# Kernel optimization log

Hardware: AMD Instinct MI355X
Metric: run time of the kernel (lower is better)

Reference implementation:

```python
import jax, jax.numpy as jnp
import numpy as np

N, D = 16384, 2048


def setup_inputs() -> dict:
    key = jax.random.key(0)
    k1, k2, k3, k4 = jax.random.split(key, 4)
    X = jax.random.normal(k1, (N, D), dtype=jnp.float32)
    keep = jax.random.uniform(k4, (N, D)) > 0.5
    X = jnp.where(keep, X, 0.0)
    A = jax.random.normal(k2, (D, D), dtype=jnp.float32)
    b = jax.random.normal(k3, (D,), dtype=jnp.float32)
    return {"X": X, "A": A, "b": b}


def reference(X, A, b):
    # y_pred = X @ A.T + b
    y_pred = jnp.einsum('nd,kd->nk', X, A) + b  # [N, D]
    mask = X != 0
    masked = jnp.where(mask, y_pred, 0.0)
    row_sum = masked.sum(axis=1, keepdims=True)          # [N, 1]
    has_any = mask.any(axis=1, keepdims=True)            # [N, 1]
    y_out = jnp.where(mask, masked / row_sum, 0.0)
    # rows with an empty mask stay all-zero (matches the Python-loop guard)
    y_out = jnp.where(has_any, y_out, 0.0)
    return y_out
```

## Files before the change

### kernel.cpp

```cpp
#include <hip/hip_runtime.h>

#define N_ROWS 16384
#define D_DIM  2048
#define BM 128
#define BN 128
#define BK 32
#define NKT (D_DIM / BK)

typedef __attribute__((ext_vector_type(8))) _Float16 half8;
typedef __attribute__((ext_vector_type(4))) _Float16 half4_t;
typedef __attribute__((ext_vector_type(4))) float floatx4;

__global__ __launch_bounds__(256, 2)
void gemm_mask_kernel(const float* __restrict__ X,
                      const float* __restrict__ A,
                      const float* __restrict__ bias,
                      float* __restrict__ out)
{
    __shared__ __align__(16) _Float16 sXh[2][BM * BK];
    __shared__ __align__(16) _Float16 sXl[2][BM * BK];
    __shared__ __align__(16) _Float16 sAh[2][BN * BK];
    __shared__ __align__(16) _Float16 sAl[2][BN * BK];

    const int t   = threadIdx.x;
    const int bid = blockIdx.x;

    const int xcd    = bid & 7;
    const int local  = bid >> 3;
    const int r_tile = (xcd << 4) + (local & 15);
    const int c_tile = local >> 4;
    const int m0 = r_tile * BM;
    const int n0 = c_tile * BN;

    const int lane  = t & 63;
    const int w     = t >> 6;
    const int wr    = w >> 1;
    const int wc    = w & 1;
    const int lrow  = lane & 15;
    const int lslot = lane >> 4;

    const float4* X4 = reinterpret_cast<const float4*>(X);
    const float4* A4 = reinterpret_cast<const float4*>(A);

    floatx4 acc1[4][4], acc2[4][4];
    #pragma unroll
    for (int mi = 0; mi < 4; ++mi)
        #pragma unroll
        for (int ni = 0; ni < 4; ++ni)
            #pragma unroll
            for (int j = 0; j < 4; ++j) { acc1[mi][ni][j] = 0.f; acc2[mi][ni][j] = 0.f; }

    float4 rx[4], ra[4];

    #pragma unroll
    for (int i = 0; i < 4; ++i) {
        int f = i * 256 + t; int row = f >> 3; int k4 = f & 7;
        rx[i] = X4[(size_t)(m0 + row) * (D_DIM / 4) + k4];
        ra[i] = A4[(size_t)(n0 + row) * (D_DIM / 4) + k4];
    }

    auto stage = [&](int buf, const float4* rv, _Float16* dsh, _Float16* dsl) {
        #pragma unroll
        for (int i = 0; i < 4; ++i) {
            int f = i * 256 + t; int row = f >> 3; int k4 = f & 7;
            float4 v = rv[i];
            half4_t h, l;
            h[0] = (_Float16)v.x; h[1] = (_Float16)v.y;
            h[2] = (_Float16)v.z; h[3] = (_Float16)v.w;
            l[0] = (_Float16)((v.x - (float)h[0]) * 4096.0f);
            l[1] = (_Float16)((v.y - (float)h[1]) * 4096.0f);
            l[2] = (_Float16)((v.z - (float)h[2]) * 4096.0f);
            l[3] = (_Float16)((v.w - (float)h[3]) * 4096.0f);
            int off = row * BK + ((((k4 >> 1) ^ ((row >> 1) & 3)) << 3) + ((k4 & 1) << 2));
            *reinterpret_cast<half4_t*>(dsh + off) = h;
            *reinterpret_cast<half4_t*>(dsl + off) = l;
        }
        (void)buf;
    };

    stage(0, rx, &sXh[0][0], &sXl[0][0]);
    stage(0, ra, &sAh[0][0], &sAl[0][0]);

    int cur = 0;
    for (int kt = 0; kt < NKT; ++kt) {
        __syncthreads();
        const bool more = (kt + 1 < NKT);
        if (more) {
            int kb = (kt + 1) * (BK / 4);
            #pragma unroll
            for (int i = 0; i < 4; ++i) {
                int f = i * 256 + t; int row = f >> 3; int k4 = f & 7;
                rx[i] = X4[(size_t)(m0 + row) * (D_DIM / 4) + kb + k4];
                ra[i] = A4[(size_t)(n0 + row) * (D_DIM / 4) + kb + k4];
            }
        }

        half8 bhf[4], blf[4];
        #pragma unroll
        for (int ni = 0; ni < 4; ++ni) {
            int row = wc * 64 + ni * 16 + lrow;
            int off = row * BK + ((lslot ^ ((row >> 1) & 3)) << 3);
            bhf[ni] = *reinterpret_cast<const half8*>(&sAh[cur][off]);
            blf[ni] = *reinterpret_cast<const half8*>(&sAl[cur][off]);
        }
        #pragma unroll
        for (int mi = 0; mi < 4; ++mi) {
            int row = wr * 64 + mi * 16 + lrow;
            int off = row * BK + ((lslot ^ ((row >> 1) & 3)) << 3);
            half8 ah = *reinterpret_cast<const half8*>(&sXh[cur][off]);
            half8 al = *reinterpret_cast<const half8*>(&sXl[cur][off]);
            #pragma unroll
            for (int ni = 0; ni < 4; ++ni) {
                acc1[mi][ni] = __builtin_amdgcn_mfma_f32_16x16x32_f16(ah, bhf[ni], acc1[mi][ni], 0, 0, 0);
                acc2[mi][ni] = __builtin_amdgcn_mfma_f32_16x16x32_f16(ah, blf[ni], acc2[mi][ni], 0, 0, 0);
                acc2[mi][ni] = __builtin_amdgcn_mfma_f32_16x16x32_f16(al, bhf[ni], acc2[mi][ni], 0, 0, 0);
            }
        }

        if (more) {
            int nxt = cur ^ 1;
            stage(nxt, rx, &sXh[nxt][0], &sXl[nxt][0]);
            stage(nxt, ra, &sAh[nxt][0], &sAl[nxt][0]);
            cur = nxt;
        }
    }

    #pragma unroll
    for (int mi = 0; mi < 4; ++mi) {
        #pragma unroll
        for (int ni = 0; ni < 4; ++ni) {
            int c = n0 + wc * 64 + ni * 16 + lrow;
            float bv = bias[c];
            #pragma unroll
            for (int j = 0; j < 4; ++j) {
                int r = m0 + wr * 64 + mi * 16 + lslot * 4 + j;
                float v = acc1[mi][ni][j] + acc2[mi][ni][j] * (1.0f / 4096.0f) + bv;
                float xv = X[(size_t)r * D_DIM + c];
                out[(size_t)r * D_DIM + c] = (xv != 0.0f) ? v : 0.0f;
            }
        }
    }
}

__global__ void row_sum_inv_kernel(const float* __restrict__ out, float* __restrict__ inv)
{
    int gw = (blockIdx.x * 256 + threadIdx.x) >> 6;
    int l  = threadIdx.x & 63;
    const float4* row = reinterpret_cast<const float4*>(out) + (size_t)gw * (D_DIM / 4);
    float s = 0.f;
    #pragma unroll
    for (int j = 0; j < 8; ++j) {
        float4 v = row[j * 64 + l];
        s += (v.x + v.y) + (v.z + v.w);
    }
    #pragma unroll
    for (int off = 32; off > 0; off >>= 1) s += __shfl_down(s, off, 64);
    if (l == 0) inv[gw] = (s != 0.0f) ? (1.0f / s) : 0.0f;
}

__global__ void scale_kernel(float* __restrict__ out, const float* __restrict__ inv)
{
    const int total = N_ROWS * (D_DIM / 4);
    float4* o = reinterpret_cast<float4*>(out);
    for (int i = blockIdx.x * blockDim.x + threadIdx.x; i < total;
         i += gridDim.x * blockDim.x) {
        float s  = inv[i >> 9];
        float4 v = o[i];
        v.x *= s; v.y *= s; v.z *= s; v.w *= s;
        o[i] = v;
    }
}

extern "C" void kernel_launch(void* const* d_in, const int* in_sizes, int n_in,
                              void* d_out, int out_size, void* d_ws, size_t ws_size,
                              hipStream_t stream)
{
    const float* X  = (const float*)d_in[0];
    const float* A  = (const float*)d_in[1];
    const float* b  = (const float*)d_in[2];
    float* out = (float*)d_out;
    float* inv = (float*)d_ws;

    hipLaunchKernelGGL(gemm_mask_kernel, dim3((N_ROWS / BM) * (D_DIM / BN)), dim3(256), 0, stream,
                       X, A, b, out);
    hipLaunchKernelGGL(row_sum_inv_kernel, dim3(N_ROWS / 4), dim3(256), 0, stream, out, inv);
    hipLaunchKernelGGL(scale_kernel, dim3(2048), dim3(256), 0, stream, out, inv);
}
```

Measured before the change: 493.8 us.

## Pre-split operands into fp16 hi/lo buffers and load tiles directly to LDS

Adds a pre-pass kernel that splits X and A into fp16 high and scaled-low halves in workspace. The GEMM then streams these directly into shared memory with global_load_lds, one wave per operand buffer, removing the per-tile fp32-to-fp16 conversion and register staging from the main loop. The cost is an extra full read of X and A plus writes of the split copies, and the path only runs if the workspace is large enough (about 150 MB); otherwise the old kernel runs.

After: 533.5 us. 1.08x slower.

```diff
diff --git a/kernel.cpp b/kernel.cpp
--- a/kernel.cpp
+++ b/kernel.cpp
@@ -11,11 +11,39 @@
 typedef __attribute__((ext_vector_type(4))) _Float16 half4_t;
 typedef __attribute__((ext_vector_type(4))) float floatx4;
 
+typedef __attribute__((address_space(1))) const unsigned int as1_uint;
+typedef __attribute__((address_space(3))) unsigned int as3_uint;
+
+__device__ __forceinline__ void gload_lds16(const _Float16* g, _Float16* l) {
+    __builtin_amdgcn_global_load_lds((as1_uint*)g, (as3_uint*)l, 16, 0, 0);
+}
+
+__global__ void split_kernel(const float4* __restrict__ src,
+                             half4_t* __restrict__ dh,
+                             half4_t* __restrict__ dl, int count4)
+{
+    for (int i = blockIdx.x * blockDim.x + threadIdx.x; i < count4;
+         i += gridDim.x * blockDim.x) {
+        float4 v = src[i];
+        half4_t h, l;
+        h[0] = (_Float16)v.x; h[1] = (_Float16)v.y;
+        h[2] = (_Float16)v.z; h[3] = (_Float16)v.w;
+        l[0] = (_Float16)((v.x - (float)h[0]) * 4096.0f);
+        l[1] = (_Float16)((v.y - (float)h[1]) * 4096.0f);
+        l[2] = (_Float16)((v.z - (float)h[2]) * 4096.0f);
+        l[3] = (_Float16)((v.w - (float)h[3]) * 4096.0f);
+        dh[i] = h; dl[i] = l;
+    }
+}
+
 __global__ __launch_bounds__(256, 2)
-void gemm_mask_kernel(const float* __restrict__ X,
-                      const float* __restrict__ A,
-                      const float* __restrict__ bias,
-                      float* __restrict__ out)
+void gemm_presplit_kernel(const _Float16* __restrict__ Xh,
+                          const _Float16* __restrict__ Xl,
+                          const _Float16* __restrict__ Ah,
+                          const _Float16* __restrict__ Al,
+                          const float* __restrict__ X,
+                          const float* __restrict__ bias,
+                          float* __restrict__ out)
 {
     __shared__ __align__(16) _Float16 sXh[2][BM * BK];
     __shared__ __align__(16) _Float16 sXl[2][BM * BK];
@@ -39,6 +67,114 @@
     const int lrow  = lane & 15;
     const int lslot = lane >> 4;
 
+    floatx4 acc1[4][4], acc2[4][4];
+    #pragma unroll
+    for (int mi = 0; mi < 4; ++mi)
+        #pragma unroll
+        for (int ni = 0; ni < 4; ++ni)
+            #pragma unroll
+            for (int j = 0; j < 4; ++j) { acc1[mi][ni][j] = 0.f; acc2[mi][ni][j] = 0.f; }
+
+    const _Float16* gsrc;
+    _Float16* lb0; _Float16* lb1;
+    if      (w == 0) { gsrc = Xh + (size_t)m0 * D_DIM; lb0 = &sXh[0][0]; lb1 = &sXh[1][0]; }
+    else if (w == 1) { gsrc = Xl + (size_t)m0 * D_DIM; lb0 = &sXl[0][0]; lb1 = &sXl[1][0]; }
+    else if (w == 2) { gsrc = Ah + (size_t)n0 * D_DIM; lb0 = &sAh[0][0]; lb1 = &sAh[1][0]; }
+    else             { gsrc = Al + (size_t)n0 * D_DIM; lb0 = &sAl[0][0]; lb1 = &sAl[1][0]; }
+
+    int off8[8];
+    #pragma unroll
+    for (int i = 0; i < 8; ++i) {
+        int c = i * 64 + lane;
+        int row = c >> 2;
+        int sp  = c & 3;
+        int kslot = sp ^ ((row >> 1) & 3);
+        off8[i] = row * D_DIM + kslot * 8;
+    }
+
+    auto issue = [&](int buf, int kt) {
+        _Float16* lb = buf ? lb1 : lb0;
+        const _Float16* gk = gsrc + kt * BK;
+        #pragma unroll
+        for (int i = 0; i < 8; ++i)
+            gload_lds16(gk + off8[i], lb + i * 512);
+    };
+
+    issue(0, 0);
+
+    int cur = 0;
+    for (int kt = 0; kt < NKT; ++kt) {
+        __syncthreads();
+        if (kt + 1 < NKT) issue(cur ^ 1, kt + 1);
+
+        half8 bhf[4], blf[4];
+        #pragma unroll
+        for (int ni = 0; ni < 4; ++ni) {
+            int row = wc * 64 + ni * 16 + lrow;
+            int off = row * BK + ((lslot ^ ((row >> 1) & 3)) << 3);
+            bhf[ni] = *reinterpret_cast<const half8*>(&sAh[cur][off]);
+            blf[ni] = *reinterpret_cast<const half8*>(&sAl[cur][off]);
+        }
+        #pragma unroll
+        for (int mi = 0; mi < 4; ++mi) {
+            int row = wr * 64 + mi * 16 + lrow;
+            int off = row * BK + ((lslot ^ ((row >> 1) & 3)) << 3);
+            half8 ah = *reinterpret_cast<const half8*>(&sXh[cur][off]);
+            half8 al = *reinterpret_cast<const half8*>(&sXl[cur][off]);
+            #pragma unroll
+            for (int ni = 0; ni < 4; ++ni) {
+                acc1[mi][ni] = __builtin_amdgcn_mfma_f32_16x16x32_f16(ah, bhf[ni], acc1[mi][ni], 0, 0, 0);
+                acc2[mi][ni] = __builtin_amdgcn_mfma_f32_16x16x32_f16(ah, blf[ni], acc2[mi][ni], 0, 0, 0);
+                acc2[mi][ni] = __builtin_amdgcn_mfma_f32_16x16x32_f16(al, bhf[ni], acc2[mi][ni], 0, 0, 0);
+            }
+        }
+        cur ^= 1;
+    }
+
+    #pragma unroll
+    for (int mi = 0; mi < 4; ++mi) {
+        #pragma unroll
+        for (int ni = 0; ni < 4; ++ni) {
+            int c = n0 + wc * 64 + ni * 16 + lrow;
+            float bv = bias[c];
+            #pragma unroll
+            for (int j = 0; j < 4; ++j) {
+                int r = m0 + wr * 64 + mi * 16 + lslot * 4 + j;
+                float v = acc1[mi][ni][j] + acc2[mi][ni][j] * (1.0f / 4096.0f) + bv;
+                float xv = X[(size_t)r * D_DIM + c];
+                out[(size_t)r * D_DIM + c] = (xv != 0.0f) ? v : 0.0f;
+            }
+        }
+    }
+}
+
+__global__ __launch_bounds__(256, 2)
+void gemm_mask_kernel(const float* __restrict__ X,
+                      const float* __restrict__ A,
+                      const float* __restrict__ bias,
+                      float* __restrict__ out)
+{
+    __shared__ __align__(16) _Float16 sXh[2][BM * BK];
+    __shared__ __align__(16) _Float16 sXl[2][BM * BK];
+    __shared__ __align__(16) _Float16 sAh[2][BN * BK];
+    __shared__ __align__(16) _Float16 sAl[2][BN * BK];
+
+    const int t   = threadIdx.x;
+    const int bid = blockIdx.x;
+    const int xcd    = bid & 7;
+    const int local  = bid >> 3;
+    const int r_tile = (xcd << 4) + (local & 15);
+    const int c_tile = local >> 4;
+    const int m0 = r_tile * BM;
+    const int n0 = c_tile * BN;
+
+    const int lane  = t & 63;
+    const int w     = t >> 6;
+    const int wr    = w >> 1;
+    const int wc    = w & 1;
+    const int lrow  = lane & 15;
+    const int lslot = lane >> 4;
+
     const float4* X4 = reinterpret_cast<const float4*>(X);
     const float4* A4 = reinterpret_cast<const float4*>(A);
 
@@ -51,7 +187,6 @@
             for (int j = 0; j < 4; ++j) { acc1[mi][ni][j] = 0.f; acc2[mi][ni][j] = 0.f; }
 
     float4 rx[4], ra[4];
-
     #pragma unroll
     for (int i = 0; i < 4; ++i) {
         int f = i * 256 + t; int row = f >> 3; int k4 = f & 7;
@@ -59,7 +194,7 @@
         ra[i] = A4[(size_t)(n0 + row) * (D_DIM / 4) + k4];
     }
 
-    auto stage = [&](int buf, const float4* rv, _Float16* dsh, _Float16* dsl) {
+    auto stage = [&](const float4* rv, _Float16* dsh, _Float16* dsl) {
         #pragma unroll
         for (int i = 0; i < 4; ++i) {
             int f = i * 256 + t; int row = f >> 3; int k4 = f & 7;
@@ -75,11 +210,10 @@
             *reinterpret_cast<half4_t*>(dsh + off) = h;
             *reinterpret_cast<half4_t*>(dsl + off) = l;
         }
-        (void)buf;
     };
 
-    stage(0, rx, &sXh[0][0], &sXl[0][0]);
-    stage(0, ra, &sAh[0][0], &sAl[0][0]);
+    stage(rx, &sXh[0][0], &sXl[0][0]);
+    stage(ra, &sAh[0][0], &sAl[0][0]);
 
     int cur = 0;
     for (int kt = 0; kt < NKT; ++kt) {
@@ -119,8 +253,8 @@
 
         if (more) {
             int nxt = cur ^ 1;
-            stage(nxt, rx, &sXh[nxt][0], &sXl[nxt][0]);
-            stage(nxt, ra, &sAh[nxt][0], &sAl[nxt][0]);
+            stage(rx, &sXh[nxt][0], &sXl[nxt][0]);
+            stage(ra, &sAh[nxt][0], &sAl[nxt][0]);
             cur = nxt;
         }
     }
@@ -179,10 +313,32 @@
     const float* A  = (const float*)d_in[1];
     const float* b  = (const float*)d_in[2];
     float* out = (float*)d_out;
-    float* inv = (float*)d_ws;
-
-    hipLaunchKernelGGL(gemm_mask_kernel, dim3((N_ROWS / BM) * (D_DIM / BN)), dim3(256), 0, stream,
-                       X, A, b, out);
-    hipLaunchKernelGGL(row_sum_inv_kernel, dim3(N_ROWS / 4), dim3(256), 0, stream, out, inv);
-    hipLaunchKernelGGL(scale_kernel, dim3(2048), dim3(256), 0, stream, out, inv);
-}
+
+    const size_t nX = (size_t)N_ROWS * D_DIM;
+    const size_t nA = (size_t)D_DIM * D_DIM;
+    const size_t inv_bytes  = (size_t)N_ROWS * sizeof(float);
+    const size_t need = inv_bytes + 2 * nX * 2 + 2 * nA * 2;
+
+    if (ws_size >= need) {
+        float*    inv = (float*)d_ws;
+        _Float16* Xh  = (_Float16*)((char*)d_ws + inv_bytes);
+        _Float16* Xl  = Xh + nX;
+        _Float16* Ah  = Xl + nX;
+        _Float16* Al  = Ah + nA;
+
+        hipLaunchKernelGGL(split_kernel, dim3(4096), dim3(256), 0, stream,
+                           (const float4*)X, (half4_t*)Xh, (half4_t*)Xl, (int)(nX / 4));
+        hipLaunchKernelGGL(split_kernel, dim3(1024), dim3(256), 0, stream,
+                           (const float4*)A, (half4_t*)Ah, (half4_t*)Al, (int)(nA / 4));
+        hipLaunchKernelGGL(gemm_presplit_kernel, dim3((N_ROWS / BM) * (D_DIM / BN)), dim3(256), 0, stream,
+                           Xh, Xl, Ah, Al, X, b, out);
+        hipLaunchKernelGGL(row_sum_inv_kernel, dim3(N_ROWS / 4), dim3(256), 0, stream, out, inv);
+        hipLaunchKernelGGL(scale_kernel, dim3(2048), dim3(256), 0, stream, out, inv);
+    } else {
+        float* inv = (float*)d_ws;
+        hipLaunchKernelGGL(gemm_mask_kernel, dim3((N_ROWS / BM) * (D_DIM / BN)), dim3(256), 0, stream,
+                           X, A, b, out);
+        hipLaunchKernelGGL(row_sum_inv_kernel, dim3(N_ROWS / 4), dim3(256), 0, stream, out, inv);
+        hipLaunchKernelGGL(scale_kernel, dim3(2048), dim3(256), 0, stream, out, inv);
+    }
+}
```
